# Kernel tuning notes

Measured on AMD Instinct MI355X. Metric: run time of the kernel, lower is better.

Reference implementation:

```python
import jax, jax.numpy as jnp
import numpy as np
import math

EMBED_DIM = 1024
NUM_HEADS = 4
HEAD_DIM = EMBED_DIM // NUM_HEADS
B, N = 4, 2048


def setup_inputs() -> dict:
    key = jax.random.key(0)
    ks = jax.random.split(key, 5)
    s = 1.0 / math.sqrt(EMBED_DIM)
    return {
        "x": jax.random.normal(ks[0], (B, N, EMBED_DIM), dtype=jnp.float32),
        "w_qkv": jax.random.normal(ks[1], (EMBED_DIM, 3 * EMBED_DIM), dtype=jnp.float32) * s,
        "b_qkv": jnp.zeros((3 * EMBED_DIM,), dtype=jnp.float32),
        "w_out": jax.random.normal(ks[2], (EMBED_DIM, EMBED_DIM), dtype=jnp.float32) * s,
        "b_out": jnp.zeros((EMBED_DIM,), dtype=jnp.float32),
        "ln_gamma": jnp.ones((EMBED_DIM,), dtype=jnp.float32),
        "ln_beta": jnp.zeros((EMBED_DIM,), dtype=jnp.float32),
    }


def reference(x, w_qkv, b_qkv, w_out, b_out, ln_gamma, ln_beta):
    Bx, Nx, D = x.shape
    qkv = x @ w_qkv + b_qkv  # [B, N, 3D]
    q, k, v = jnp.split(qkv, 3, axis=-1)
    # [B, H, N, hd]
    def heads(t):
        return t.reshape(Bx, Nx, NUM_HEADS, HEAD_DIM).transpose(0, 2, 1, 3)
    q, k, v = heads(q), heads(k), heads(v)
    scale = 1.0 / math.sqrt(HEAD_DIM)
    attn = jnp.einsum("bhqd,bhkd->bhqk", q, k) * scale  # [B, H, N, N]
    attn = jax.nn.softmax(attn, axis=-1)
    out = jnp.einsum("bhqk,bhkd->bhqd", attn, v)  # [B, H, N, hd]
    out = out.transpose(0, 2, 1, 3).reshape(Bx, Nx, D)
    out = out @ w_out + b_out
    # residual + LayerNorm (eps=1e-5 like torch default)
    y = x + out
    mu = jnp.mean(y, axis=-1, keepdims=True)
    var = jnp.mean(jnp.square(y - mu), axis=-1, keepdims=True)
    y = (y - mu) * jax.lax.rsqrt(var + 1e-5)
    return y * ln_gamma + ln_beta
```

## Files before the change

kernel.cpp:

```cpp
#include <hip/hip_runtime.h>
#include <hip/hip_bf16.h>

typedef __attribute__((ext_vector_type(8))) short short8;
typedef __attribute__((ext_vector_type(4))) float f32x4;
typedef __attribute__((ext_vector_type(16))) float f32x16;
typedef __attribute__((ext_vector_type(4))) unsigned uint4v;

#define GLOB_AS __attribute__((address_space(1)))
#define LDS_AS  __attribute__((address_space(3)))

__device__ __forceinline__ void async16(void* lds, const void* g) {
  __builtin_amdgcn_global_load_lds((const GLOB_AS unsigned int*)g,
                                   (LDS_AS unsigned int*)lds, 16, 0, 0);
}

__device__ __forceinline__ unsigned short f2bf(float f) {
  unsigned u = __float_as_uint(f);
  unsigned r = u + 0x7FFFu + ((u >> 16) & 1u);
  return (unsigned short)(r >> 16);
}

__device__ __forceinline__ float bf2f(unsigned short u) {
  unsigned x = ((unsigned)u) << 16;
  return __uint_as_float(x);
}

__device__ __forceinline__ unsigned pk2(float lo, float hi) {
  __hip_bfloat162 h = __float22bfloat162_rn(float2{lo, hi});
  return *reinterpret_cast<unsigned*>(&h);
}

__device__ __forceinline__ void lane32_swap(unsigned& a, unsigned& b, int lane) {
#if __has_builtin(__builtin_amdgcn_permlane32_swap)
  auto r = __builtin_amdgcn_permlane32_swap(a, b, false, false);
  a = r[0]; b = r[1];
#else
  unsigned tb = __shfl_xor(b, 32);
  unsigned ta = __shfl_xor(a, 32);
  unsigned na = (lane < 32) ? a : tb;
  unsigned nb = (lane < 32) ? ta : b;
  a = na; b = nb;
#endif
}

#define BATCH 4
#define SEQ   2048
#define DMODEL 1024
#define NHEAD 4
#define HD    256

#define QSCALE 0.090169944f
#define DEFER_THR 11.5f

__global__ __launch_bounds__(256) void cast_bf16_kernel(
    const float* __restrict__ in, unsigned short* __restrict__ out) {
  int i = blockIdx.x * 256 + threadIdx.x;
  float4 v = ((const float4*)in)[i];
  uint2 o;
  o.x = (unsigned)f2bf(v.x) | ((unsigned)f2bf(v.y) << 16);
  o.y = (unsigned)f2bf(v.z) | ((unsigned)f2bf(v.w) << 16);
  ((uint2*)out)[i] = o;
}

__global__ __launch_bounds__(256) void transpose_cast_kernel(
    const float* __restrict__ in, unsigned short* __restrict__ out, int R, int C) {
  __shared__ float tile[32][33];
  int c0 = blockIdx.x * 32, r0 = blockIdx.y * 32;
  int tx = threadIdx.x, ty = threadIdx.y;
#pragma unroll
  for (int i = 0; i < 4; ++i)
    tile[ty + 8 * i][tx] = in[(size_t)(r0 + ty + 8 * i) * C + c0 + tx];
  __syncthreads();
#pragma unroll
  for (int i = 0; i < 4; ++i)
    out[(size_t)(c0 + ty + 8 * i) * R + r0 + tx] = f2bf(tile[tx][ty + 8 * i]);
}

__global__ __launch_bounds__(256) void gemm_qkv_kernel(
    const unsigned short* __restrict__ A,
    const unsigned short* __restrict__ Bt,
    const float* __restrict__ bias,
    unsigned short* __restrict__ qb,
    unsigned short* __restrict__ kb,
    unsigned short* __restrict__ vt) {
  __shared__ __align__(16) unsigned short sA[2][128 * 32];
  __shared__ __align__(16) unsigned short sB[2][128 * 32];
  const int t = threadIdx.x;
  const int l = t & 63, w = t >> 6;
  const int g = l >> 4, lr = l & 15;
  const int wr = w >> 1, wc = w & 1;
  const int row0 = blockIdx.y * 128;
  const int col0 = blockIdx.x * 128;

  auto stage = [&](int buf, int kt) {
#pragma unroll
    for (int i = 0; i < 2; ++i) {
      int e = i * 256 + t;
      async16(&sA[buf][e * 8], A + (size_t)(row0 + (e >> 2)) * 1024 + kt + (e & 3) * 8);
      async16(&sB[buf][e * 8], Bt + (size_t)(col0 + (e >> 2)) * 1024 + kt + (e & 3) * 8);
    }
  };

  stage(0, 0);

  f32x4 acc[4][4] = {};
  for (int ki = 0; ki < 32; ++ki) {
    const int cur = ki & 1;
    __syncthreads();
    if (ki < 31) stage(cur ^ 1, (ki + 1) * 32);
    short8 af[4], bf[4];
#pragma unroll
    for (int m = 0; m < 4; ++m)
      af[m] = *(const short8*)&sA[cur][(wr * 64 + m * 16 + lr) * 32 + g * 8];
#pragma unroll
    for (int n = 0; n < 4; ++n)
      bf[n] = *(const short8*)&sB[cur][(wc * 64 + n * 16 + lr) * 32 + g * 8];
    __builtin_amdgcn_s_setprio(1);
#pragma unroll
    for (int m = 0; m < 4; ++m)
#pragma unroll
      for (int n = 0; n < 4; ++n)
        acc[m][n] = __builtin_amdgcn_mfma_f32_16x16x32_bf16(af[m], bf[n], acc[m][n], 0, 0, 0);
    __builtin_amdgcn_s_setprio(0);
  }

#pragma unroll
  for (int m = 0; m < 4; ++m) {
    int rowb = row0 + wr * 64 + m * 16 + g * 4;
    int b = rowb >> 11;
    int nb = rowb & 2047;
#pragma unroll
    for (int nn = 0; nn < 4; ++nn) {
      int col = col0 + wc * 64 + nn * 16 + lr;
      float bv = bias[col];
      int sec = col >> 10, c1 = col & 1023;
      int h = c1 >> 8, d = c1 & 255;
      if (sec == 2) {
        unsigned short p0 = f2bf(acc[m][nn][0] + bv);
        unsigned short p1 = f2bf(acc[m][nn][1] + bv);
        unsigned short p2 = f2bf(acc[m][nn][2] + bv);
        unsigned short p3 = f2bf(acc[m][nn][3] + bv);
        uint2 pk;
        pk.x = (unsigned)p0 | ((unsigned)p1 << 16);
        pk.y = (unsigned)p2 | ((unsigned)p3 << 16);
        size_t idx = (((size_t)((b * NHEAD + h) * 128 + (nb >> 4))) * 256 + d) * 16 + (nb & 15);
        *(uint2*)&vt[idx] = pk;
      } else {
        unsigned short* dst = (sec == 0) ? qb : kb;
        float sc = (sec == 0) ? QSCALE : 1.0f;
#pragma unroll
        for (int rr = 0; rr < 4; ++rr) {
          size_t idx = ((size_t)((b * NHEAD + h) * SEQ + nb + rr)) * HD + d;
          dst[idx] = f2bf((acc[m][nn][rr] + bv) * sc);
        }
      }
    }
  }
}

__global__ __launch_bounds__(256, 2) void attn_kernel(
    const unsigned short* __restrict__ qb,
    const unsigned short* __restrict__ kb,
    const unsigned short* __restrict__ vt,
    unsigned short* __restrict__ Oh,
    float2* __restrict__ st) {
  __shared__ __align__(16) unsigned short sK[2][32 * 256];
  __shared__ __align__(16) unsigned short sV[2][2 * 256 * 16];
  const int t = threadIdx.x, l = t & 63, w = t >> 6;
  const int row = l & 31, hi = l >> 5;
  const int swz = row << 4;
  const int bid = blockIdx.x;
  const int bh = (bid & 7) * 2 + ((bid >> 3) & 1);
  const int qblk = (bid >> 4) & 15;
  const int kvhalf = bid >> 8;
  const int b = bh >> 2, h = bh & 3;
  const int q = qblk * 128 + w * 32 + row;
  const unsigned short* Qp = qb + (size_t)bh * SEQ * HD;
  const char* Kg = (const char*)(kb + (size_t)bh * SEQ * HD);
  const char* Vg = (const char*)(vt + (size_t)bh * (128 * 256 * 16));

  short8 qf[16];
#pragma unroll
  for (int dc = 0; dc < 16; ++dc)
    qf[dc] = *(const short8*)&Qp[(size_t)q * HD + dc * 16 + hi * 8];

  auto stage = [&](int buf, int kp0) {
#pragma unroll
    for (int i = 0; i < 4; ++i) {
      int s = i * 256 + t;
      int r = s >> 5;
      int colb = (s & 31) * 16;
      int src = (kp0 + r) * 512 + (colb ^ (r << 4));
      async16((char*)sK[buf] + s * 16, Kg + src);
    }
    const int c0 = kp0 >> 4;
#pragma unroll
    for (int i = 0; i < 4; ++i) {
      int s = i * 256 + t;
      int kh = s >> 9, rem = s & 511;
      int d = rem >> 1, vhi = rem & 1;
      int src = ((c0 + kh) * 256 + d) * 32 + vhi * 16;
      async16((char*)sV[buf] + s * 16, Vg + src);
    }
  };

  stage(0, kvhalf * 32);
  __syncthreads();

  f32x16 O[8] = {};
  float mrun = -__builtin_inff();
  float lsum = 0.f;

  for (int it = 0; it < 32; ++it) {
    const int kp0 = (2 * it + kvhalf) * 32;
    const int cur = it & 1;
    if (it < 31) stage(cur ^ 1, kp0 + 64);

    f32x16 Sa = {}, Sb = {};
    const char* sKc = (const char*)sK[cur];
    __builtin_amdgcn_s_setprio(1);
#pragma unroll
    for (int dc = 0; dc < 16; dc += 2) {
      short8 kf0 = *(const short8*)(sKc + row * 512 + ((dc * 32 + hi * 16) ^ swz));
      short8 kf1 = *(const short8*)(sKc + row * 512 + (((dc + 1) * 32 + hi * 16) ^ swz));
      Sa = __builtin_amdgcn_mfma_f32_32x32x16_bf16(kf0, qf[dc], Sa, 0, 0, 0);
      Sb = __builtin_amdgcn_mfma_f32_32x32x16_bf16(kf1, qf[dc + 1], Sb, 0, 0, 0);
    }
    __builtin_amdgcn_s_setprio(0);

    float p[16];
#pragma unroll
    for (int i = 0; i < 16; ++i) p[i] = Sa[i] + Sb[i];
    float m0 = fmaxf(fmaxf(fmaxf(p[0], p[1]), fmaxf(p[2], p[3])),
                     fmaxf(fmaxf(p[4], p[5]), fmaxf(p[6], p[7])));
    float m1 = fmaxf(fmaxf(fmaxf(p[8], p[9]), fmaxf(p[10], p[11])),
                     fmaxf(fmaxf(p[12], p[13]), fmaxf(p[14], p[15])));
    float cmax = fmaxf(m0, m1);
    cmax = fmaxf(cmax, __shfl_xor(cmax, 32));

    if (!__all(cmax <= mrun + DEFER_THR)) {
      float mnew = fmaxf(mrun, cmax);
      float alpha = exp2f(mrun - mnew);
      lsum *= alpha;
#pragma unroll
      for (int db = 0; db < 8; ++db) O[db] *= alpha;
      mrun = mnew;
    }

    float e[16];
#pragma unroll
    for (int i = 0; i < 16; ++i) e[i] = exp2f(p[i] - mrun);
    float s0 = (e[0] + e[1]) + (e[2] + e[3]);
    float s1 = (e[4] + e[5]) + (e[6] + e[7]);
    float s2 = (e[8] + e[9]) + (e[10] + e[11]);
    float s3 = (e[12] + e[13]) + (e[14] + e[15]);
    float ps = (s0 + s1) + (s2 + s3);
    ps += __shfl_xor(ps, 32);
    lsum += ps;

    unsigned a0 = pk2(e[0], e[1]),   a1 = pk2(e[2], e[3]);
    unsigned b0 = pk2(e[4], e[5]),   b1 = pk2(e[6], e[7]);
    unsigned c0 = pk2(e[8], e[9]),   c1 = pk2(e[10], e[11]);
    unsigned d0 = pk2(e[12], e[13]), d1 = pk2(e[14], e[15]);
    lane32_swap(a0, b0, l);
    lane32_swap(a1, b1, l);
    lane32_swap(c0, d0, l);
    lane32_swap(c1, d1, l);
    uint4v u1; u1.x = a0; u1.y = a1; u1.z = b0; u1.w = b1;
    uint4v u2; u2.x = c0; u2.y = c1; u2.z = d0; u2.w = d1;
    short8 pf1 = __builtin_bit_cast(short8, u1);
    short8 pf2 = __builtin_bit_cast(short8, u2);

    const char* sVc = (const char*)sV[cur];
    __builtin_amdgcn_s_setprio(1);
#pragma unroll
    for (int db = 0; db < 8; ++db) {
      short8 vf0 = *(const short8*)(sVc + ((db * 32 + row) * 2 + hi) * 16);
      short8 vf1 = *(const short8*)(sVc + 8192 + ((db * 32 + row) * 2 + hi) * 16);
      O[db] = __builtin_amdgcn_mfma_f32_32x32x16_bf16(vf0, pf1, O[db], 0, 0, 0);
      O[db] = __builtin_amdgcn_mfma_f32_32x32x16_bf16(vf1, pf2, O[db], 0, 0, 0);
    }
    __builtin_amdgcn_s_setprio(0);

    __syncthreads();
  }

  float inv = 1.0f / lsum;
  unsigned short* aop = Oh + (size_t)kvhalf * (8192ull * 1024);
  size_t obase = ((size_t)(b * SEQ + q)) * DMODEL + h * HD;
#pragma unroll
  for (int db = 0; db < 8; ++db)
#pragma unroll
    for (int rg = 0; rg < 4; ++rg) {
      int dd = db * 32 + rg * 8 + hi * 4;
      uint2 pk;
      pk.x = pk2(O[db][rg * 4 + 0] * inv, O[db][rg * 4 + 1] * inv);
      pk.y = pk2(O[db][rg * 4 + 2] * inv, O[db][rg * 4 + 3] * inv);
      *(uint2*)&aop[obase + dd] = pk;
    }
  if (hi == 0)
    st[((size_t)kvhalf * 16 + bh) * 2048 + q] = make_float2(mrun, lsum);
}

__global__ __launch_bounds__(256) void combine_kernel(
    const unsigned short* __restrict__ Oh,
    const float2* __restrict__ st,
    unsigned short* __restrict__ ao) {
  int rowg = blockIdx.x, t = threadIdx.x;
  int b = rowg >> 11, q = rowg & 2047;
  int col = t * 4;
  int bh = b * 4 + (col >> 8);
  float2 s0 = st[(size_t)bh * 2048 + q];
  float2 s1 = st[(16ull * 2048) + (size_t)bh * 2048 + q];
  float M = fmaxf(s0.x, s1.x);
  float w0 = s0.y * exp2f(s0.x - M);
  float w1 = s1.y * exp2f(s1.x - M);
  float inv = 1.0f / (w0 + w1);
  w0 *= inv; w1 *= inv;
  size_t base = (size_t)rowg * 1024 + col;
  uint2 ua = *(const uint2*)&Oh[base];
  uint2 ub = *(const uint2*)&Oh[8192ull * 1024 + base];
  unsigned short oa[4] = {(unsigned short)(ua.x & 0xFFFF), (unsigned short)(ua.x >> 16),
                          (unsigned short)(ua.y & 0xFFFF), (unsigned short)(ua.y >> 16)};
  unsigned short ob[4] = {(unsigned short)(ub.x & 0xFFFF), (unsigned short)(ub.x >> 16),
                          (unsigned short)(ub.y & 0xFFFF), (unsigned short)(ub.y >> 16)};
  float r[4];
#pragma unroll
  for (int j = 0; j < 4; ++j) r[j] = w0 * bf2f(oa[j]) + w1 * bf2f(ob[j]);
  uint2 pk;
  pk.x = pk2(r[0], r[1]);
  pk.y = pk2(r[2], r[3]);
  *(uint2*)&ao[base] = pk;
}

__global__ __launch_bounds__(256) void gemm_out_kernel(
    const unsigned short* __restrict__ A,
    const unsigned short* __restrict__ Bt,
    const float* __restrict__ bias,
    const float* __restrict__ x,
    float* __restrict__ y) {
  __shared__ __align__(16) unsigned short sA[2][128 * 32];
  __shared__ __align__(16) unsigned short sB[2][128 * 32];
  const int t = threadIdx.x;
  const int l = t & 63, w = t >> 6;
  const int g = l >> 4, lr = l & 15;
  const int wr = w >> 1, wc = w & 1;
  const int row0 = blockIdx.y * 128;
  const int col0 = blockIdx.x * 128;

  auto stage = [&](int buf, int kt) {
#pragma unroll
    for (int i = 0; i < 2; ++i) {
      int e = i * 256 + t;
      async16(&sA[buf][e * 8], A + (size_t)(row0 + (e >> 2)) * 1024 + kt + (e & 3) * 8);
      async16(&sB[buf][e * 8], Bt + (size_t)(col0 + (e >> 2)) * 1024 + kt + (e & 3) * 8);
    }
  };

  stage(0, 0);

  f32x4 acc[4][4] = {};
  for (int ki = 0; ki < 32; ++ki) {
    const int cur = ki & 1;
    __syncthreads();
    if (ki < 31) stage(cur ^ 1, (ki + 1) * 32);
    short8 af[4], bf[4];
#pragma unroll
    for (int m = 0; m < 4; ++m)
      af[m] = *(const short8*)&sA[cur][(wr * 64 + m * 16 + lr) * 32 + g * 8];
#pragma unroll
    for (int n = 0; n < 4; ++n)
      bf[n] = *(const short8*)&sB[cur][(wc * 64 + n * 16 + lr) * 32 + g * 8];
    __builtin_amdgcn_s_setprio(1);
#pragma unroll
    for (int m = 0; m < 4; ++m)
#pragma unroll
      for (int n = 0; n < 4; ++n)
        acc[m][n] = __builtin_amdgcn_mfma_f32_16x16x32_bf16(af[m], bf[n], acc[m][n], 0, 0, 0);
    __builtin_amdgcn_s_setprio(0);
  }

#pragma unroll
  for (int m = 0; m < 4; ++m) {
    int rowb = row0 + wr * 64 + m * 16 + g * 4;
#pragma unroll
    for (int nn = 0; nn < 4; ++nn) {
      int col = col0 + wc * 64 + nn * 16 + lr;
      float bv = bias[col];
#pragma unroll
      for (int rr = 0; rr < 4; ++rr) {
        size_t idx = (size_t)(rowb + rr) * 1024 + col;
        y[idx] = acc[m][nn][rr] + bv + x[idx];
      }
    }
  }
}

__global__ __launch_bounds__(256) void ln_kernel(
    const float* __restrict__ y, const float* __restrict__ gamma,
    const float* __restrict__ beta, float* __restrict__ out) {
  int row = blockIdx.x, t = threadIdx.x;
  float4 v = ((const float4*)(y + (size_t)row * 1024))[t];
  float s = v.x + v.y + v.z + v.w;
  float qs = v.x * v.x + v.y * v.y + v.z * v.z + v.w * v.w;
#pragma unroll
  for (int off = 1; off < 64; off <<= 1) {
    s += __shfl_xor(s, off);
    qs += __shfl_xor(qs, off);
  }
  __shared__ float ss[4], qq[4];
  if ((t & 63) == 0) { ss[t >> 6] = s; qq[t >> 6] = qs; }
  __syncthreads();
  s = ss[0] + ss[1] + ss[2] + ss[3];
  qs = qq[0] + qq[1] + qq[2] + qq[3];
  float mean = s * (1.0f / 1024.0f);
  float var = qs * (1.0f / 1024.0f) - mean * mean;
  float rstd = rsqrtf(var + 1e-5f);
  float4 gm = ((const float4*)gamma)[t];
  float4 bt = ((const float4*)beta)[t];
  float4 o;
  o.x = (v.x - mean) * rstd * gm.x + bt.x;
  o.y = (v.y - mean) * rstd * gm.y + bt.y;
  o.z = (v.z - mean) * rstd * gm.z + bt.z;
  o.w = (v.w - mean) * rstd * gm.w + bt.w;
  ((float4*)(out + (size_t)row * 1024))[t] = o;
}

extern "C" void kernel_launch(void* const* d_in, const int* in_sizes, int n_in,
                              void* d_out, int out_size, void* d_ws, size_t ws_size,
                              hipStream_t stream) {
  const float* x      = (const float*)d_in[0];
  const float* w_qkv  = (const float*)d_in[1];
  const float* b_qkv  = (const float*)d_in[2];
  const float* w_out  = (const float*)d_in[3];
  const float* b_out  = (const float*)d_in[4];
  const float* gamma  = (const float*)d_in[5];
  const float* beta   = (const float*)d_in[6];
  float* out = (float*)d_out;

  char* ws = (char*)d_ws;
  unsigned short* xb    = (unsigned short*)(ws);
  unsigned short* wqkvT = (unsigned short*)(ws + (16u << 20));
  unsigned short* woutT = (unsigned short*)(ws + (22u << 20));
  unsigned short* qb    = (unsigned short*)(ws + (24u << 20));
  unsigned short* kb    = (unsigned short*)(ws + (40u << 20));
  unsigned short* vt    = (unsigned short*)(ws + (56u << 20));
  unsigned short* ao    = (unsigned short*)(ws + (72u << 20));
  unsigned short* Oh    = (unsigned short*)(ws + (88u << 20));
  float* y              = (float*)(ws + (88u << 20));
  float2* st            = (float2*)(ws + (16u << 20));

  cast_bf16_kernel<<<(BATCH * SEQ * DMODEL) / (256 * 4), 256, 0, stream>>>(x, xb);
  transpose_cast_kernel<<<dim3(96, 32), dim3(32, 8), 0, stream>>>(w_qkv, wqkvT, 1024, 3072);
  transpose_cast_kernel<<<dim3(32, 32), dim3(32, 8), 0, stream>>>(w_out, woutT, 1024, 1024);
  gemm_qkv_kernel<<<dim3(24, 64), 256, 0, stream>>>(xb, wqkvT, b_qkv, qb, kb, vt);
  attn_kernel<<<512, 256, 0, stream>>>(qb, kb, vt, Oh, st);
  combine_kernel<<<BATCH * SEQ, 256, 0, stream>>>(Oh, st, ao);
  gemm_out_kernel<<<dim3(8, 64), 256, 0, stream>>>(ao, woutT, b_out, x, y);
  ln_kernel<<<BATCH * SEQ, 256, 0, stream>>>(y, gamma, beta, out);
}
```

Baseline: 248.9 us.

## Remap GEMM blocks for XCD-local weight reuse and store pre-LN residual in bf16

Both GEMMs now use a 1D grid. Block ids are remapped so that each of the 8 XCDs (blocks assigned round-robin) works on its own column slice of the weight matrix, which should improve L2 reuse of the B operand. The output GEMM now writes the residual sum y as bf16 instead of fp32, and the LayerNorm kernel reads bf16. This halves the intermediate write and read traffic but reduces the precision of the LayerNorm input.

```diff
diff --git a/kernel.cpp b/kernel.cpp
--- a/kernel.cpp
+++ b/kernel.cpp
@@ -89,8 +89,11 @@
   const int l = t & 63, w = t >> 6;
   const int g = l >> 4, lr = l & 15;
   const int wr = w >> 1, wc = w & 1;
-  const int row0 = blockIdx.y * 128;
-  const int col0 = blockIdx.x * 128;
+  const int bid = blockIdx.x;
+  const int xcd = bid & 7, sub = bid >> 3;
+  const int bxl = sub % 3, by = sub / 3;
+  const int row0 = by * 128;
+  const int col0 = (xcd * 3 + bxl) * 128;
 
   auto stage = [&](int buf, int kt) {
 #pragma unroll
@@ -338,15 +341,17 @@
     const unsigned short* __restrict__ Bt,
     const float* __restrict__ bias,
     const float* __restrict__ x,
-    float* __restrict__ y) {
+    unsigned short* __restrict__ y) {
   __shared__ __align__(16) unsigned short sA[2][128 * 32];
   __shared__ __align__(16) unsigned short sB[2][128 * 32];
   const int t = threadIdx.x;
   const int l = t & 63, w = t >> 6;
   const int g = l >> 4, lr = l & 15;
   const int wr = w >> 1, wc = w & 1;
-  const int row0 = blockIdx.y * 128;
-  const int col0 = blockIdx.x * 128;
+  const int bid = blockIdx.x;
+  const int xcd = bid & 7, by = bid >> 3;
+  const int row0 = by * 128;
+  const int col0 = xcd * 128;
 
   auto stage = [&](int buf, int kt) {
 #pragma unroll
@@ -390,19 +395,23 @@
 #pragma unroll
       for (int rr = 0; rr < 4; ++rr) {
         size_t idx = (size_t)(rowb + rr) * 1024 + col;
-        y[idx] = acc[m][nn][rr] + bv + x[idx];
+        y[idx] = f2bf(acc[m][nn][rr] + bv + x[idx]);
       }
     }
   }
 }
 
 __global__ __launch_bounds__(256) void ln_kernel(
-    const float* __restrict__ y, const float* __restrict__ gamma,
+    const unsigned short* __restrict__ y, const float* __restrict__ gamma,
     const float* __restrict__ beta, float* __restrict__ out) {
   int row = blockIdx.x, t = threadIdx.x;
-  float4 v = ((const float4*)(y + (size_t)row * 1024))[t];
-  float s = v.x + v.y + v.z + v.w;
-  float qs = v.x * v.x + v.y * v.y + v.z * v.z + v.w * v.w;
+  uint2 u = ((const uint2*)(y + (size_t)row * 1024))[t];
+  float v0 = bf2f((unsigned short)(u.x & 0xFFFF));
+  float v1 = bf2f((unsigned short)(u.x >> 16));
+  float v2 = bf2f((unsigned short)(u.y & 0xFFFF));
+  float v3 = bf2f((unsigned short)(u.y >> 16));
+  float s = v0 + v1 + v2 + v3;
+  float qs = v0 * v0 + v1 * v1 + v2 * v2 + v3 * v3;
 #pragma unroll
   for (int off = 1; off < 64; off <<= 1) {
     s += __shfl_xor(s, off);
@@ -419,10 +428,10 @@
   float4 gm = ((const float4*)gamma)[t];
   float4 bt = ((const float4*)beta)[t];
   float4 o;
-  o.x = (v.x - mean) * rstd * gm.x + bt.x;
-  o.y = (v.y - mean) * rstd * gm.y + bt.y;
-  o.z = (v.z - mean) * rstd * gm.z + bt.z;
-  o.w = (v.w - mean) * rstd * gm.w + bt.w;
+  o.x = (v0 - mean) * rstd * gm.x + bt.x;
+  o.y = (v1 - mean) * rstd * gm.y + bt.y;
+  o.z = (v2 - mean) * rstd * gm.z + bt.z;
+  o.w = (v3 - mean) * rstd * gm.w + bt.w;
   ((float4*)(out + (size_t)row * 1024))[t] = o;
 }
 
@@ -447,15 +456,15 @@
   unsigned short* vt    = (unsigned short*)(ws + (56u << 20));
   unsigned short* ao    = (unsigned short*)(ws + (72u << 20));
   unsigned short* Oh    = (unsigned short*)(ws + (88u << 20));
-  float* y              = (float*)(ws + (88u << 20));
+  unsigned short* y     = (unsigned short*)(ws + (88u << 20));
   float2* st            = (float2*)(ws + (16u << 20));
 
   cast_bf16_kernel<<<(BATCH * SEQ * DMODEL) / (256 * 4), 256, 0, stream>>>(x, xb);
   transpose_cast_kernel<<<dim3(96, 32), dim3(32, 8), 0, stream>>>(w_qkv, wqkvT, 1024, 3072);
   transpose_cast_kernel<<<dim3(32, 32), dim3(32, 8), 0, stream>>>(w_out, woutT, 1024, 1024);
-  gemm_qkv_kernel<<<dim3(24, 64), 256, 0, stream>>>(xb, wqkvT, b_qkv, qb, kb, vt);
+  gemm_qkv_kernel<<<1536, 256, 0, stream>>>(xb, wqkvT, b_qkv, qb, kb, vt);
   attn_kernel<<<512, 256, 0, stream>>>(qb, kb, vt, Oh, st);
   combine_kernel<<<BATCH * SEQ, 256, 0, stream>>>(Oh, st, ao);
-  gemm_out_kernel<<<dim3(8, 64), 256, 0, stream>>>(ao, woutT, b_out, x, y);
+  gemm_out_kernel<<<512, 256, 0, stream>>>(ao, woutT, b_out, x, y);
   ln_kernel<<<BATCH * SEQ, 256, 0, stream>>>(y, gamma, beta, out);
 }
```

Result: no change. 246.7 us (-0.9%).
